# Kernel tuning notes

Measured on AMD Instinct MI355X. Metric: run time of the kernel, lower is better.

The kernel has to match this reference:

```python
import jax, jax.numpy as jnp
import numpy as np

N_ITEMS = 100000
HIDDEN = 128
N_EDGES = 1600000


def setup_inputs() -> dict:
    key = jax.random.key(0)
    k1, k2, k3, k4 = jax.random.split(key, 4)
    item_emb = jax.random.normal(k1, (N_ITEMS, HIDDEN), dtype=jnp.float32) * 0.02
    adj_rows = jax.random.randint(k2, (N_EDGES,), 0, N_ITEMS, dtype=jnp.int32)
    adj_cols = jax.random.randint(k3, (N_EDGES,), 0, N_ITEMS, dtype=jnp.int32)
    adj_vals = jax.random.uniform(k4, (N_EDGES,), dtype=jnp.float32)
    return {
        "item_emb": item_emb,
        "adj_rows": adj_rows,
        "adj_cols": adj_cols,
        "adj_vals": adj_vals,
        "num_layers": 3,
    }


def _spmm(rows, cols, vals, embeds, n_rows):
    # y[r] = sum_{e: rows[e]==r} vals[e] * embeds[cols[e]]  (COO spmm)
    gathered = embeds[cols] * vals[:, None]  # [E, H]
    return jax.ops.segment_sum(gathered, rows, num_segments=n_rows)


def reference(item_emb, adj_rows, adj_cols, adj_vals, num_layers):
    embeds = [item_emb]
    for _ in range(num_layers):
        embeds.append(_spmm(adj_rows, adj_cols, adj_vals, embeds[-1], item_emb.shape[0]))
    # sum over all layer embeddings (running-sum aggregation)
    total = embeds[0]
    for e in embeds[1:]:
        total = total + e
    return (total, jnp.stack(embeds, axis=0))
```

## Files before the change

kernel.cpp:

```cpp
#include <hip/hip_runtime.h>
#include <hip/hip_fp16.h>

#define HIDDEN 128
#define SCAN_TILE 1024
#define SCAN_BLOCK 256

typedef float cvec4 __attribute__((ext_vector_type(4)));

__device__ inline void nt_store4(float4* p, float4 v) {
    cvec4 x; x.x = v.x; x.y = v.y; x.z = v.z; x.w = v.w;
    __builtin_nontemporal_store(x, reinterpret_cast<cvec4*>(p));
}
__device__ inline float4 nt_load4(const float4* p) {
    cvec4 x = __builtin_nontemporal_load(reinterpret_cast<const cvec4*>(p));
    return make_float4(x.x, x.y, x.z, x.w);
}

__global__ void zero_counts(int* __restrict__ counts, int n) {
    int i = blockIdx.x * blockDim.x + threadIdx.x;
    int stride = gridDim.x * blockDim.x;
    for (; i < n; i += stride) counts[i] = 0;
}

__global__ void hist_kernel(const int* __restrict__ rows,
                            int* __restrict__ counts,
                            int* __restrict__ rank,
                            int E) {
    int i = blockIdx.x * blockDim.x + threadIdx.x;
    int stride = gridDim.x * blockDim.x;
    for (; i < E; i += stride) rank[i] = atomicAdd(&counts[rows[i]], 1);
}

__global__ void scan_partial_sums(const int* __restrict__ counts,
                                  int* __restrict__ block_sums,
                                  int n) {
    __shared__ int sdata[SCAN_BLOCK];
    int t = threadIdx.x;
    int idx = blockIdx.x * SCAN_TILE + t * 4;
    int s = 0;
    if (idx + 3 < n) {
        int4 c = *reinterpret_cast<const int4*>(counts + idx);
        s = c.x + c.y + c.z + c.w;
    } else if (idx < n) {
        s = counts[idx];
        if (idx + 1 < n) s += counts[idx + 1];
        if (idx + 2 < n) s += counts[idx + 2];
    }
    sdata[t] = s;
    __syncthreads();
    for (int off = SCAN_BLOCK / 2; off > 0; off >>= 1) {
        if (t < off) sdata[t] += sdata[t + off];
        __syncthreads();
    }
    if (t == 0) block_sums[blockIdx.x] = sdata[0];
}

__global__ void scan_block_offsets(int* __restrict__ block_sums,
                                   int* __restrict__ row_ptr,
                                   int nb, int n) {
    __shared__ int sdata[SCAN_BLOCK];
    int t = threadIdx.x;
    int chunk = (nb + SCAN_BLOCK - 1) / SCAN_BLOCK;
    int lo = t * chunk;
    int hi = min(lo + chunk, nb);
    int s = 0;
    for (int i = lo; i < hi; ++i) s += block_sums[i];
    sdata[t] = s;
    __syncthreads();
    for (int off = 1; off < SCAN_BLOCK; off <<= 1) {
        int u = (t >= off) ? sdata[t - off] : 0;
        __syncthreads();
        sdata[t] += u;
        __syncthreads();
    }
    int run = sdata[t] - s;
    for (int i = lo; i < hi; ++i) {
        int v = block_sums[i];
        block_sums[i] = run;
        run += v;
    }
    if (t == SCAN_BLOCK - 1) row_ptr[n] = sdata[SCAN_BLOCK - 1];
}

__global__ void scan_apply(const int* __restrict__ counts,
                           const int* __restrict__ block_offsets,
                           int* __restrict__ row_ptr,
                           int n) {
    __shared__ int sdata[SCAN_BLOCK];
    int t = threadIdx.x;
    int idx = blockIdx.x * SCAN_TILE + t * 4;
    int v0 = 0, v1 = 0, v2 = 0, v3 = 0;
    if (idx + 3 < n) {
        int4 c = *reinterpret_cast<const int4*>(counts + idx);
        v0 = c.x; v1 = c.y; v2 = c.z; v3 = c.w;
    } else if (idx < n) {
        v0 = counts[idx];
        if (idx + 1 < n) v1 = counts[idx + 1];
        if (idx + 2 < n) v2 = counts[idx + 2];
    }
    int s = v0 + v1 + v2 + v3;
    sdata[t] = s;
    __syncthreads();
    for (int off = 1; off < SCAN_BLOCK; off <<= 1) {
        int u = (t >= off) ? sdata[t - off] : 0;
        __syncthreads();
        sdata[t] += u;
        __syncthreads();
    }
    int run = sdata[t] - s + block_offsets[blockIdx.x];
    if (idx < n)     { row_ptr[idx]     = run; run += v0; }
    if (idx + 1 < n) { row_ptr[idx + 1] = run; run += v1; }
    if (idx + 2 < n) { row_ptr[idx + 2] = run; run += v2; }
    if (idx + 3 < n) { row_ptr[idx + 3] = run; run += v3; }
}

__global__ void scatter_kernel(const int* __restrict__ rows,
                               const int* __restrict__ cols,
                               const float* __restrict__ vals,
                               const int* __restrict__ row_ptr,
                               const int* __restrict__ rank,
                               int2* __restrict__ colval,
                               int E) {
    int i = blockIdx.x * blockDim.x + threadIdx.x;
    int stride = gridDim.x * blockDim.x;
    for (; i < E; i += stride) {
        int pos = row_ptr[rows[i]] + rank[i];
        colval[pos] = make_int2(cols[i], __float_as_int(vals[i]));
    }
}

__global__ void convert_copy(const float4* __restrict__ src,
                             float4* __restrict__ s0,
                             float4* __restrict__ xh,
                             size_t n8) {
    size_t stride = (size_t)gridDim.x * blockDim.x;
    for (size_t i = (size_t)blockIdx.x * blockDim.x + threadIdx.x; i < n8; i += stride) {
        float4 a = nt_load4(src + i * 2);
        float4 b = nt_load4(src + i * 2 + 1);
        nt_store4(s0 + i * 2, a);
        nt_store4(s0 + i * 2 + 1, b);
        __half2 h[4];
        h[0] = __floats2half2_rn(a.x, a.y);
        h[1] = __floats2half2_rn(a.z, a.w);
        h[2] = __floats2half2_rn(b.x, b.y);
        h[3] = __floats2half2_rn(b.z, b.w);
        xh[i] = *reinterpret_cast<float4*>(h);
    }
}

template <bool WRITE_SHADOW>
__global__ void spmm_h16(const int* __restrict__ row_ptr,
                         const int2* __restrict__ colval,
                         const float4* __restrict__ xh,
                         float* __restrict__ y,
                         float4* __restrict__ yh,
                         int n_rows) {
    int tid = (int)((size_t)blockIdx.x * blockDim.x + threadIdx.x);
    int row = tid >> 4;
    int li  = threadIdx.x & 15;
    if (row >= n_rows) return;

    int start = row_ptr[row];
    int end   = row_ptr[row + 1];

    float acc[8] = {0.f, 0.f, 0.f, 0.f, 0.f, 0.f, 0.f, 0.f};

    for (int base = start; base < end; base += 16) {
        int idx = base + li;
        int c = 0; float v = 0.f;
        if (idx < end) {
            int2 cv = colval[idx];
            c = cv.x;
            v = __int_as_float(cv.y);
        }
        int n = min(16, end - base);

        float4 h[16];
        #pragma unroll
        for (int j = 0; j < 16; ++j) {
            int cj = __shfl(c, j, 16);
            if (j < n) h[j] = xh[(size_t)cj * 16 + li];
        }

        #pragma unroll
        for (int j = 0; j < 16; ++j) {
            if (j < n) {
                float vj = __shfl(v, j, 16);
                const __half2* hp = reinterpret_cast<const __half2*>(&h[j]);
                float2 f0 = __half22float2(hp[0]);
                float2 f1 = __half22float2(hp[1]);
                float2 f2 = __half22float2(hp[2]);
                float2 f3 = __half22float2(hp[3]);
                acc[0] += vj * f0.x; acc[1] += vj * f0.y;
                acc[2] += vj * f1.x; acc[3] += vj * f1.y;
                acc[4] += vj * f2.x; acc[5] += vj * f2.y;
                acc[6] += vj * f3.x; acc[7] += vj * f3.y;
            }
        }
    }

    size_t ob = (size_t)row * 32 + (size_t)(li * 2);
    nt_store4((float4*)y + ob,     make_float4(acc[0], acc[1], acc[2], acc[3]));
    nt_store4((float4*)y + ob + 1, make_float4(acc[4], acc[5], acc[6], acc[7]));

    if (WRITE_SHADOW) {
        __half2 h2[4];
        h2[0] = __floats2half2_rn(acc[0], acc[1]);
        h2[1] = __floats2half2_rn(acc[2], acc[3]);
        h2[2] = __floats2half2_rn(acc[4], acc[5]);
        h2[3] = __floats2half2_rn(acc[6], acc[7]);
        yh[(size_t)row * 16 + li] = *reinterpret_cast<float4*>(h2);
    }
}

__global__ void total_kernel(const float4* __restrict__ s0,
                             const float4* __restrict__ s1,
                             const float4* __restrict__ s2,
                             const float4* __restrict__ s3,
                             float4* __restrict__ t,
                             size_t n4) {
    size_t stride = (size_t)gridDim.x * blockDim.x;
    for (size_t i = (size_t)blockIdx.x * blockDim.x + threadIdx.x; i < n4; i += stride) {
        float4 a = nt_load4(s0 + i), b = nt_load4(s1 + i);
        float4 c = nt_load4(s2 + i), d = nt_load4(s3 + i);
        float4 o;
        o.x = a.x + b.x + c.x + d.x;
        o.y = a.y + b.y + c.y + d.y;
        o.z = a.z + b.z + c.z + d.z;
        o.w = a.w + b.w + c.w + d.w;
        nt_store4(t + i, o);
    }
}

extern "C" void kernel_launch(void* const* d_in, const int* in_sizes, int n_in,
                              void* d_out, int out_size, void* d_ws, size_t ws_size,
                              hipStream_t stream) {
    const float* item_emb = (const float*)d_in[0];
    const int*   adj_rows = (const int*)d_in[1];
    const int*   adj_cols = (const int*)d_in[2];
    const float* adj_vals = (const float*)d_in[3];

    const size_t NH = (size_t)in_sizes[0];
    const int    E  = in_sizes[1];
    const int    N  = (int)(NH / HIDDEN);

    float* T  = (float*)d_out;
    float* S0 = T + NH;
    float* S1 = S0 + NH;
    float* S2 = S1 + NH;
    float* S3 = S2 + NH;

    float4* shA  = (float4*)T;
    float4* shB  = (float4*)S3;
    int*    rank = (int*)S1;

    char* ws = (char*)d_ws;
    int*   row_ptr = (int*)ws;                       ws += ((size_t)(N + 1) * 4 + 15) & ~15ull;
    int*   counts  = (int*)ws;                       ws += ((size_t)N * 4 + 15) & ~15ull;
    int2*  colval  = (int2*)ws;

    const int nb = (N + SCAN_TILE - 1) / SCAN_TILE;
    int* block_sums = (int*)(colval + E) - nb;

    {
        int block = 256;
        int gridN = min((N + block - 1) / block, 4096);
        int gridE = min((E + block - 1) / block, 8192);
        zero_counts<<<gridN, block, 0, stream>>>(counts, N);
        hist_kernel<<<gridE, block, 0, stream>>>(adj_rows, counts, rank, E);
        scan_partial_sums<<<nb, SCAN_BLOCK, 0, stream>>>(counts, block_sums, N);
        scan_block_offsets<<<1, SCAN_BLOCK, 0, stream>>>(block_sums, row_ptr, nb, N);
        scan_apply<<<nb, SCAN_BLOCK, 0, stream>>>(counts, block_sums, row_ptr, N);
        scatter_kernel<<<gridE, block, 0, stream>>>(adj_rows, adj_cols, adj_vals,
                                                    row_ptr, rank, colval, E);
    }

    {
        size_t n8 = NH / 8;
        int block = 256;
        int grid = (int)min((n8 + block - 1) / block, (size_t)8192);
        convert_copy<<<grid, block, 0, stream>>>((const float4*)item_emb,
                                                 (float4*)S0, shA, n8);
    }

    {
        int block = 256;
        int grid = (N * 16 + block - 1) / block;
        spmm_h16<true><<<grid, block, 0, stream>>>(row_ptr, colval, shA, S1, shB, N);
        spmm_h16<true><<<grid, block, 0, stream>>>(row_ptr, colval, shB, S2, shA, N);
        spmm_h16<false><<<grid, block, 0, stream>>>(row_ptr, colval, shA, S3, nullptr, N);
    }

    {
        size_t n4 = NH / 4;
        int block = 256;
        int grid = (int)min((n4 + block - 1) / block, (size_t)8192);
        total_kernel<<<grid, block, 0, stream>>>((const float4*)S0, (const float4*)S1,
                                                 (const float4*)S2, (const float4*)S3,
                                                 (float4*)T, n4);
    }
}
```

Measured before the change: 628.5 us.

## Sort rows by degree so SpMM warps process similar-length rows

Adds a degree histogram, a scan and a scatter that build a row permutation grouped by clamped row degree. The SpMM kernels then map each 16-lane group to a row through that permutation, so rows in the same wavefront have similar lengths and less divergence. The cost is four extra small kernels with atomics, one extra indirection per row, and output writes that become scattered rather than sequential.

```diff
diff --git a/kernel.cpp b/kernel.cpp
--- a/kernel.cpp
+++ b/kernel.cpp
@@ -112,6 +112,47 @@
     if (idx + 1 < n) { row_ptr[idx + 1] = run; run += v1; }
     if (idx + 2 < n) { row_ptr[idx + 2] = run; run += v2; }
     if (idx + 3 < n) { row_ptr[idx + 3] = run; run += v3; }
+}
+
+__global__ void deg_zero(int* __restrict__ bins) {
+    if (threadIdx.x < 128) bins[threadIdx.x] = 0;
+}
+
+__global__ void deg_hist(const int* __restrict__ row_ptr,
+                         int* __restrict__ bins, int n) {
+    int i = blockIdx.x * blockDim.x + threadIdx.x;
+    int stride = gridDim.x * blockDim.x;
+    for (; i < n; i += stride) {
+        int d = min(row_ptr[i + 1] - row_ptr[i], 63);
+        atomicAdd(&bins[d], 1);
+    }
+}
+
+__global__ void deg_scan(const int* __restrict__ bins,
+                         int* __restrict__ cursors) {
+    __shared__ int sdata[64];
+    int t = threadIdx.x;
+    sdata[t] = bins[t];
+    __syncthreads();
+    for (int off = 1; off < 64; off <<= 1) {
+        int u = (t >= off) ? sdata[t - off] : 0;
+        __syncthreads();
+        sdata[t] += u;
+        __syncthreads();
+    }
+    cursors[t] = sdata[t] - bins[t];
+}
+
+__global__ void deg_scatter(const int* __restrict__ row_ptr,
+                            int* __restrict__ cursors,
+                            int* __restrict__ row_order, int n) {
+    int i = blockIdx.x * blockDim.x + threadIdx.x;
+    int stride = gridDim.x * blockDim.x;
+    for (; i < n; i += stride) {
+        int d = min(row_ptr[i + 1] - row_ptr[i], 63);
+        int pos = atomicAdd(&cursors[d], 1);
+        row_order[pos] = i;
+    }
 }
 
 __global__ void scatter_kernel(const int* __restrict__ rows,
@@ -150,15 +191,17 @@
 
 template <bool WRITE_SHADOW>
 __global__ void spmm_h16(const int* __restrict__ row_ptr,
+                         const int* __restrict__ row_order,
                          const int2* __restrict__ colval,
                          const float4* __restrict__ xh,
                          float* __restrict__ y,
                          float4* __restrict__ yh,
                          int n_rows) {
     int tid = (int)((size_t)blockIdx.x * blockDim.x + threadIdx.x);
-    int row = tid >> 4;
+    int slot = tid >> 4;
     int li  = threadIdx.x & 15;
-    if (row >= n_rows) return;
+    if (slot >= n_rows) return;
+    int row = row_order[slot];
 
     int start = row_ptr[row];
     int end   = row_ptr[row + 1];
@@ -253,11 +296,15 @@
     float4* shA  = (float4*)T;
     float4* shB  = (float4*)S3;
     int*    rank = (int*)S1;
+    int*    bins    = (int*)S1 + E;
+    int*    cursors = (int*)S1 + E + 64;
 
     char* ws = (char*)d_ws;
     int*   row_ptr = (int*)ws;                       ws += ((size_t)(N + 1) * 4 + 15) & ~15ull;
     int*   counts  = (int*)ws;                       ws += ((size_t)N * 4 + 15) & ~15ull;
     int2*  colval  = (int2*)ws;
+
+    int* row_order = counts;
 
     const int nb = (N + SCAN_TILE - 1) / SCAN_TILE;
     int* block_sums = (int*)(colval + E) - nb;
@@ -271,6 +318,10 @@
         scan_partial_sums<<<nb, SCAN_BLOCK, 0, stream>>>(counts, block_sums, N);
         scan_block_offsets<<<1, SCAN_BLOCK, 0, stream>>>(block_sums, row_ptr, nb, N);
         scan_apply<<<nb, SCAN_BLOCK, 0, stream>>>(counts, block_sums, row_ptr, N);
+        deg_zero<<<1, 128, 0, stream>>>(bins);
+        deg_hist<<<gridN, block, 0, stream>>>(row_ptr, bins, N);
+        deg_scan<<<1, 64, 0, stream>>>(bins, cursors);
+        deg_scatter<<<gridN, block, 0, stream>>>(row_ptr, cursors, row_order, N);
         scatter_kernel<<<gridE, block, 0, stream>>>(adj_rows, adj_cols, adj_vals,
                                                     row_ptr, rank, colval, E);
     }
@@ -286,9 +337,9 @@
     {
         int block = 256;
         int grid = (N * 16 + block - 1) / block;
-        spmm_h16<true><<<grid, block, 0, stream>>>(row_ptr, colval, shA, S1, shB, N);
-        spmm_h16<true><<<grid, block, 0, stream>>>(row_ptr, colval, shB, S2, shA, N);
-        spmm_h16<false><<<grid, block, 0, stream>>>(row_ptr, colval, shA, S3, nullptr, N);
+        spmm_h16<true><<<grid, block, 0, stream>>>(row_ptr, row_order, colval, shA, S1, shB, N);
+        spmm_h16<true><<<grid, block, 0, stream>>>(row_ptr, row_order, colval, shB, S2, shA, N);
+        spmm_h16<false><<<grid, block, 0, stream>>>(row_ptr, row_order, colval, shA, S3, nullptr, N);
     }
 
     {
```

Result: slower. 1.178 ms (+87.5%).
